# Optimization experiments

Hardware: AMD Instinct MI355X
Metric: run time of the kernel (lower is better)

Reference implementation:

```python
import jax, jax.numpy as jnp
import numpy as np
from itertools import combinations

N_COLS = 16   # number of input features (columns of xl/xu)
ADD = 3       # max subset order
ALPHA = 0.5   # primary compare weight
BETA = 0.8    # tie-break compare weight
BATCH = 65536


def _bitmask(combo):
    m = 0
    for i in combo:
        m |= 1 << i
    return m


def _build_plan(n, add):
    """Static DP plan: for each subset length, gather indices of combo[1:] (left)
    and combo[:-1] (right) among previously computed columns; plus final bitmask order."""
    items = list(range(n))
    index_dict = {(i,): i for i in items}
    count = n
    plan = []
    for length in range(2, min(add, n) + 1):
        combos = list(combinations(items, length))
        if not combos:
            continue
        left = np.array([index_dict[c[1:]] for c in combos], dtype=np.int32)
        right = np.array([index_dict[c[:-1]] for c in combos], dtype=np.int32)
        for c in combos:
            index_dict[c] = count
            count += 1
        plan.append((left, right))
    order = np.array([index_dict[c] for c in sorted(index_dict, key=_bitmask)], dtype=np.int32)
    return plan, order

_PLAN, _ORDER = _build_plan(N_COLS, ADD)


def setup_inputs() -> dict:
    key = jax.random.key(0)
    k1, k2 = jax.random.split(key)
    a = jax.random.uniform(k1, (BATCH, N_COLS), dtype=jnp.float32)
    b = jax.random.uniform(k2, (BATCH, N_COLS), dtype=jnp.float32)
    # valid intervals: xl <= xu elementwise
    xl = jnp.minimum(a, b)
    xu = jnp.maximum(a, b)
    return {"xl": xl, "xu": xu}


def _select_pair(ll, lu, rl, ru):
    # alpha-weighted score; pick the interval with SMALLER score (choose_right when cur > nxt)
    cur = (1.0 - ALPHA) * ll + ALPHA * lu
    nxt = (1.0 - ALPHA) * rl + ALPHA * ru
    # tie-break with beta-weighted score
    beta_cur = (1.0 - BETA) * ll + BETA * lu
    beta_nxt = (1.0 - BETA) * rl + BETA * ru
    choose_right = jnp.where(cur == nxt, beta_cur > beta_nxt, cur > nxt)
    res_l = jnp.where(choose_right, rl, ll)
    res_u = jnp.where(choose_right, ru, lu)
    return res_l, res_u


def reference(xl, xu):
    # mat_* grow by one block per subset length; gathers use static index arrays
    mat_l, mat_u = xl, xu
    for left_idx, right_idx in _PLAN:
        ll = mat_l[:, left_idx]
        lu = mat_u[:, left_idx]
        rl = mat_l[:, right_idx]
        ru = mat_u[:, right_idx]
        res_l, res_u = _select_pair(ll, lu, rl, ru)
        mat_l = jnp.concatenate([mat_l, res_l], axis=1)
        mat_u = jnp.concatenate([mat_u, res_u], axis=1)
    # reorder columns by subset bitmask, as in _reorder_by_bitmask
    return mat_l[:, _ORDER], mat_u[:, _ORDER]
```

## Files before the change

### kernel.cpp

```cpp
#include <hip/hip_runtime.h>
#include <cstdint>

#define NCOLS  696
#define NGROUP 174
#define NREC   136
#define WPB    4
#define BLOCK  256
#define GRID   2048
#define ROWS_PER_WAVE 8

typedef float v4f __attribute__((ext_vector_type(4)));

constexpr int pr(int a, int b) { return 16 + b * (b - 1) / 2 + a; }

struct alignas(8) RecSrc { uint16_t d[NREC]; };
constexpr RecSrc make_recs() {
    RecSrc t{};
    for (int a = 0; a < 16; ++a) t.d[a] = (uint16_t)(a | (a << 8));
    int p = 16;
    for (int b = 1; b < 16; ++b)
        for (int a = 0; a < b; ++a)
            t.d[p++] = (uint16_t)(a | (b << 8));
    return t;
}

struct alignas(8) ColTbl { uint16_t d[NCOLS]; };
constexpr ColTbl make_cols() {
    ColTbl t{};
    int p = 0;
    for (int h = 0; h < 16; ++h) {
        t.d[p++] = (uint16_t)(h | (h << 8));
        for (int j = 0; j < h; ++j) {
            int pjh = pr(j, h);
            t.d[p++] = (uint16_t)(pjh | (pjh << 8));
            for (int i = 0; i < j; ++i)
                t.d[p++] = (uint16_t)(pr(j, h) | (pr(i, j) << 8));
        }
    }
    return t;
}

__constant__ RecSrc g_recs = make_recs();
__constant__ ColTbl g_cols = make_cols();

__device__ __forceinline__ float2 selpair(float2 L, float2 R) {
    float curL = __fadd_rn(L.x, L.y);
    float curR = __fadd_rn(R.x, R.y);
    float bL = __fadd_rn(__fmul_rn(0.2f, L.x), __fmul_rn(0.8f, L.y));
    float bR = __fadd_rn(__fmul_rn(0.2f, R.x), __fmul_rn(0.8f, R.y));
    bool choose_right = (curL == curR) ? (bL > bR) : (curL > curR);
    return choose_right ? R : L;
}

__device__ __forceinline__ float2 col_compute(const float2* __restrict__ rec,
                                              uint32_t d) {
    float2 L = rec[d & 255u];
    float2 R = rec[(d >> 8) & 255u];
    return selpair(L, R);
}

__global__ __launch_bounds__(BLOCK) void minint_kernel(
    const float* __restrict__ xl, const float* __restrict__ xu,
    float* __restrict__ out, int batch)
{
    __shared__ float2 vals[WPB][16];
    __shared__ float2 recs[WPB][NREC];
    const int t    = threadIdx.x;
    const int w    = t >> 6;
    const int lane = t & 63;
    const int wgid = blockIdx.x * WPB + w;

    float2* v   = vals[w];
    float2* rec = recs[w];
    const ushort4* cols = (const ushort4*)g_cols.d;

    for (int it = 0; it < ROWS_PER_WAVE; ++it) {
        const int row = wgid * ROWS_PER_WAVE + it;
        if (row >= batch) break;

        if (lane < 32) {
            const float* src = (lane < 16) ? (xl + (size_t)row * 16 + lane)
                                           : (xu + (size_t)row * 16 + (lane - 16));
            ((float*)v)[(lane & 15) * 2 + (lane >> 4)] = *src;
        }

        #pragma unroll
        for (int m = 0; m < 3; ++m) {
            int r = lane + 64 * m;
            if (r < NREC) {
                uint32_t s = g_recs.d[r];
                float2 lo = v[s & 15u];
                float2 hi = v[(s >> 8) & 15u];
                rec[r] = selpair(hi, lo);
            }
        }

        float* outl = out + (size_t)row * NCOLS;
        float* outu = out + (size_t)batch * NCOLS + (size_t)row * NCOLS;

        #pragma unroll
        for (int k = 0; k < 3; ++k) {
            int g = lane + 64 * k;
            if (g < NGROUP) {
                ushort4 d4 = cols[g];
                float2 c0 = col_compute(rec, d4.x);
                float2 c1 = col_compute(rec, d4.y);
                float2 c2 = col_compute(rec, d4.z);
                float2 c3 = col_compute(rec, d4.w);
                v4f rl = { c0.x, c1.x, c2.x, c3.x };
                v4f ru = { c0.y, c1.y, c2.y, c3.y };
                __builtin_nontemporal_store(rl, (v4f*)(outl + 4 * g));
                __builtin_nontemporal_store(ru, (v4f*)(outu + 4 * g));
            }
        }
    }
}

extern "C" void kernel_launch(void* const* d_in, const int* in_sizes, int n_in,
                              void* d_out, int out_size, void* d_ws, size_t ws_size,
                              hipStream_t stream) {
    const float* xl = (const float*)d_in[0];
    const float* xu = (const float*)d_in[1];
    float* out = (float*)d_out;
    const int batch = in_sizes[0] / 16;
    minint_kernel<<<GRID, BLOCK, 0, stream>>>(xl, xu, out, batch);
}
```

Baseline: 403.3 us.

## Process one row per wave with a larger grid and hoisted LDS loads

Drops the per-wave loop over eight rows and launches one block per four rows, so each wave handles a single row. The column gathers from LDS are issued early, before the selects and stores, to increase memory-level parallelism, and a launch-bounds occupancy hint is added. The aim is better latency hiding for the store-bound output write. The cost is a much larger grid and the loss of the row-bounds check, so it assumes batch is a multiple of four.

```diff
diff --git a/kernel.cpp b/kernel.cpp
--- a/kernel.cpp
+++ b/kernel.cpp
@@ -6,8 +6,6 @@
 #define NREC   136
 #define WPB    4
 #define BLOCK  256
-#define GRID   2048
-#define ROWS_PER_WAVE 8
 
 typedef float v4f __attribute__((ext_vector_type(4)));
 
@@ -52,14 +50,7 @@
     return choose_right ? R : L;
 }
 
-__device__ __forceinline__ float2 col_compute(const float2* __restrict__ rec,
-                                              uint32_t d) {
-    float2 L = rec[d & 255u];
-    float2 R = rec[(d >> 8) & 255u];
-    return selpair(L, R);
-}
-
-__global__ __launch_bounds__(BLOCK) void minint_kernel(
+__global__ __launch_bounds__(BLOCK, 6) void minint_kernel(
     const float* __restrict__ xl, const float* __restrict__ xu,
     float* __restrict__ out, int batch)
 {
@@ -68,51 +59,84 @@
     const int t    = threadIdx.x;
     const int w    = t >> 6;
     const int lane = t & 63;
-    const int wgid = blockIdx.x * WPB + w;
+    const int row  = blockIdx.x * WPB + w;
 
     float2* v   = vals[w];
     float2* rec = recs[w];
+
+    if (lane < 32) {
+        const float* src = (lane < 16) ? (xl + (size_t)row * 16 + lane)
+                                       : (xu + (size_t)row * 16 + (lane - 16));
+        ((float*)v)[(lane & 15) * 2 + (lane >> 4)] = *src;
+    }
+
+    {
+        uint32_t s0 = g_recs.d[lane];
+        uint32_t s1 = g_recs.d[64 + lane];
+        float2 r0 = selpair(v[(s0 >> 8) & 15u], v[s0 & 15u]);
+        float2 r1 = selpair(v[(s1 >> 8) & 15u], v[s1 & 15u]);
+        rec[lane]      = r0;
+        rec[64 + lane] = r1;
+        if (lane < NREC - 128) {
+            uint32_t s2 = g_recs.d[128 + lane];
+            rec[128 + lane] = selpair(v[(s2 >> 8) & 15u], v[s2 & 15u]);
+        }
+    }
+
+    float* outl = out + (size_t)row * NCOLS;
+    float* outu = out + (size_t)batch * NCOLS + (size_t)row * NCOLS;
     const ushort4* cols = (const ushort4*)g_cols.d;
 
-    for (int it = 0; it < ROWS_PER_WAVE; ++it) {
-        const int row = wgid * ROWS_PER_WAVE + it;
-        if (row >= batch) break;
+    const bool has2 = lane < (NGROUP - 128);
+    ushort4 d0 = cols[lane];
+    ushort4 d1 = cols[64 + lane];
+    ushort4 d2 = cols[has2 ? (128 + lane) : lane];
 
-        if (lane < 32) {
-            const float* src = (lane < 16) ? (xl + (size_t)row * 16 + lane)
-                                           : (xu + (size_t)row * 16 + (lane - 16));
-            ((float*)v)[(lane & 15) * 2 + (lane >> 4)] = *src;
-        }
+    float2 L00 = rec[d0.x & 255u], R00 = rec[d0.x >> 8];
+    float2 L01 = rec[d0.y & 255u], R01 = rec[d0.y >> 8];
+    float2 L02 = rec[d0.z & 255u], R02 = rec[d0.z >> 8];
+    float2 L03 = rec[d0.w & 255u], R03 = rec[d0.w >> 8];
+    float2 L10 = rec[d1.x & 255u], R10 = rec[d1.x >> 8];
+    float2 L11 = rec[d1.y & 255u], R11 = rec[d1.y >> 8];
+    float2 L12 = rec[d1.z & 255u], R12 = rec[d1.z >> 8];
+    float2 L13 = rec[d1.w & 255u], R13 = rec[d1.w >> 8];
 
-        #pragma unroll
-        for (int m = 0; m < 3; ++m) {
-            int r = lane + 64 * m;
-            if (r < NREC) {
-                uint32_t s = g_recs.d[r];
-                float2 lo = v[s & 15u];
-                float2 hi = v[(s >> 8) & 15u];
-                rec[r] = selpair(hi, lo);
-            }
-        }
+    {
+        float2 c0 = selpair(L00, R00);
+        float2 c1 = selpair(L01, R01);
+        float2 c2 = selpair(L02, R02);
+        float2 c3 = selpair(L03, R03);
+        v4f rl = { c0.x, c1.x, c2.x, c3.x };
+        v4f ru = { c0.y, c1.y, c2.y, c3.y };
+        __builtin_nontemporal_store(rl, (v4f*)(outl + 4 * lane));
+        __builtin_nontemporal_store(ru, (v4f*)(outu + 4 * lane));
+    }
 
-        float* outl = out + (size_t)row * NCOLS;
-        float* outu = out + (size_t)batch * NCOLS + (size_t)row * NCOLS;
+    float2 L20 = rec[d2.x & 255u], R20 = rec[d2.x >> 8];
+    float2 L21 = rec[d2.y & 255u], R21 = rec[d2.y >> 8];
+    float2 L22 = rec[d2.z & 255u], R22 = rec[d2.z >> 8];
+    float2 L23 = rec[d2.w & 255u], R23 = rec[d2.w >> 8];
 
-        #pragma unroll
-        for (int k = 0; k < 3; ++k) {
-            int g = lane + 64 * k;
-            if (g < NGROUP) {
-                ushort4 d4 = cols[g];
-                float2 c0 = col_compute(rec, d4.x);
-                float2 c1 = col_compute(rec, d4.y);
-                float2 c2 = col_compute(rec, d4.z);
-                float2 c3 = col_compute(rec, d4.w);
-                v4f rl = { c0.x, c1.x, c2.x, c3.x };
-                v4f ru = { c0.y, c1.y, c2.y, c3.y };
-                __builtin_nontemporal_store(rl, (v4f*)(outl + 4 * g));
-                __builtin_nontemporal_store(ru, (v4f*)(outu + 4 * g));
-            }
-        }
+    {
+        float2 c0 = selpair(L10, R10);
+        float2 c1 = selpair(L11, R11);
+        float2 c2 = selpair(L12, R12);
+        float2 c3 = selpair(L13, R13);
+        v4f rl = { c0.x, c1.x, c2.x, c3.x };
+        v4f ru = { c0.y, c1.y, c2.y, c3.y };
+        __builtin_nontemporal_store(rl, (v4f*)(outl + 4 * (64 + lane)));
+        __builtin_nontemporal_store(ru, (v4f*)(outu + 4 * (64 + lane)));
+    }
+
+    if (has2) {
+        float2 c0 = selpair(L20, R20);
+        float2 c1 = selpair(L21, R21);
+        float2 c2 = selpair(L22, R22);
+        float2 c3 = selpair(L23, R23);
+        v4f rl = { c0.x, c1.x, c2.x, c3.x };
+        v4f ru = { c0.y, c1.y, c2.y, c3.y };
+        __builtin_nontemporal_store(rl, (v4f*)(outl + 4 * (128 + lane)));
+        __builtin_nontemporal_store(ru, (v4f*)(outu + 4 * (128 + lane)));
     }
 }
 
@@ -123,5 +147,6 @@
     const float* xu = (const float*)d_in[1];
     float* out = (float*)d_out;
     const int batch = in_sizes[0] / 16;
-    minint_kernel<<<GRID, BLOCK, 0, stream>>>(xl, xu, out, batch);
+    const int grid  = batch / WPB;
+    minint_kernel<<<grid, BLOCK, 0, stream>>>(xl, xu, out, batch);
 }
```

Result: faster. 381.6 us (-5.4%).

## Launch one row per wave with XCD-aware block remapping and plain stores

Applied to the files above, without the earlier changes.

Replaces the persistent loop of eight rows per wave with one row per wave, launching batch/4 blocks. Block IDs are remapped by swizzling the low three bits so consecutive rows go to the same XCD, and the nontemporal stores become regular stores. The aim is better latency hiding through more waves, and better L2/write locality per XCD. The swizzle hardcodes 2048 groups per XCD and drops the row bounds check, so it is only correct for batch=65536.

```diff
diff --git a/kernel.cpp b/kernel.cpp
--- a/kernel.cpp
+++ b/kernel.cpp
@@ -6,8 +6,6 @@
 #define NREC   136
 #define WPB    4
 #define BLOCK  256
-#define GRID   2048
-#define ROWS_PER_WAVE 8
 
 typedef float v4f __attribute__((ext_vector_type(4)));
 
@@ -68,50 +66,49 @@
     const int t    = threadIdx.x;
     const int w    = t >> 6;
     const int lane = t & 63;
-    const int wgid = blockIdx.x * WPB + w;
+    const int bid  = blockIdx.x;
+    const int grp  = ((bid & 7) << 11) | (bid >> 3);
+    const int row  = grp * WPB + w;
 
     float2* v   = vals[w];
     float2* rec = recs[w];
+
+    if (lane < 32) {
+        const float* src = (lane < 16) ? (xl + (size_t)row * 16 + lane)
+                                       : (xu + (size_t)row * 16 + (lane - 16));
+        ((float*)v)[(lane & 15) * 2 + (lane >> 4)] = *src;
+    }
+
+    {
+        uint32_t s0 = g_recs.d[lane];
+        uint32_t s1 = g_recs.d[64 + lane];
+        float2 r0 = selpair(v[(s0 >> 8) & 15u], v[s0 & 15u]);
+        float2 r1 = selpair(v[(s1 >> 8) & 15u], v[s1 & 15u]);
+        rec[lane]      = r0;
+        rec[64 + lane] = r1;
+        if (lane < NREC - 128) {
+            uint32_t s2 = g_recs.d[128 + lane];
+            rec[128 + lane] = selpair(v[(s2 >> 8) & 15u], v[s2 & 15u]);
+        }
+    }
+
+    float* outl = out + (size_t)row * NCOLS;
+    float* outu = out + (size_t)batch * NCOLS + (size_t)row * NCOLS;
     const ushort4* cols = (const ushort4*)g_cols.d;
 
-    for (int it = 0; it < ROWS_PER_WAVE; ++it) {
-        const int row = wgid * ROWS_PER_WAVE + it;
-        if (row >= batch) break;
-
-        if (lane < 32) {
-            const float* src = (lane < 16) ? (xl + (size_t)row * 16 + lane)
-                                           : (xu + (size_t)row * 16 + (lane - 16));
-            ((float*)v)[(lane & 15) * 2 + (lane >> 4)] = *src;
-        }
-
-        #pragma unroll
-        for (int m = 0; m < 3; ++m) {
-            int r = lane + 64 * m;
-            if (r < NREC) {
-                uint32_t s = g_recs.d[r];
-                float2 lo = v[s & 15u];
-                float2 hi = v[(s >> 8) & 15u];
-                rec[r] = selpair(hi, lo);
-            }
-        }
-
-        float* outl = out + (size_t)row * NCOLS;
-        float* outu = out + (size_t)batch * NCOLS + (size_t)row * NCOLS;
-
-        #pragma unroll
-        for (int k = 0; k < 3; ++k) {
-            int g = lane + 64 * k;
-            if (g < NGROUP) {
-                ushort4 d4 = cols[g];
-                float2 c0 = col_compute(rec, d4.x);
-                float2 c1 = col_compute(rec, d4.y);
-                float2 c2 = col_compute(rec, d4.z);
-                float2 c3 = col_compute(rec, d4.w);
-                v4f rl = { c0.x, c1.x, c2.x, c3.x };
-                v4f ru = { c0.y, c1.y, c2.y, c3.y };
-                __builtin_nontemporal_store(rl, (v4f*)(outl + 4 * g));
-                __builtin_nontemporal_store(ru, (v4f*)(outu + 4 * g));
-            }
+    #pragma unroll
+    for (int k = 0; k < 3; ++k) {
+        int g = lane + 64 * k;
+        if (g < NGROUP) {
+            ushort4 d4 = cols[g];
+            float2 c0 = col_compute(rec, d4.x);
+            float2 c1 = col_compute(rec, d4.y);
+            float2 c2 = col_compute(rec, d4.z);
+            float2 c3 = col_compute(rec, d4.w);
+            v4f rl = { c0.x, c1.x, c2.x, c3.x };
+            v4f ru = { c0.y, c1.y, c2.y, c3.y };
+            *(v4f*)(outl + 4 * g) = rl;
+            *(v4f*)(outu + 4 * g) = ru;
         }
     }
 }
@@ -123,5 +120,6 @@
     const float* xu = (const float*)d_in[1];
     float* out = (float*)d_out;
     const int batch = in_sizes[0] / 16;
-    minint_kernel<<<GRID, BLOCK, 0, stream>>>(xl, xu, out, batch);
+    const int grid  = batch / WPB;
+    minint_kernel<<<grid, BLOCK, 0, stream>>>(xl, xu, out, batch);
 }
```

Result: faster. 377.5 us (-6.4%).
